# Kernel optimization log

Measured on AMD Instinct MI355X. Metric: run time of the kernel, lower is better.

Reference implementation:

```python
import jax, jax.numpy as jnp
import numpy as np

D_MODEL = 1024
EXPERT_DIM = 2048
N_EXPERTS = 8
LN_EPS = 1e-5


def _bit_quant(W):
    # W: [out, in] (or [..., out, in]); per-output-row ternary quantization with STE
    scale = jnp.clip(jnp.mean(jnp.abs(W), axis=-1, keepdims=True), 1e-5, None)
    w_q = jnp.clip(jnp.round(W / scale), -1.0, 1.0) * scale
    return W + jax.lax.stop_gradient(w_q - W)


def setup_inputs() -> dict:
    key = jax.random.key(0)
    ks = jax.random.split(key, 7)
    x = jax.random.normal(ks[0], (4, 2048, D_MODEL), dtype=jnp.float32)
    # kaiming_normal fan_out, linear -> std = 1/sqrt(out_features)
    shared_w1 = jax.random.normal(ks[1], (EXPERT_DIM, D_MODEL), dtype=jnp.float32) / np.sqrt(EXPERT_DIM)
    shared_w2 = jax.random.normal(ks[2], (D_MODEL, EXPERT_DIM), dtype=jnp.float32) / np.sqrt(D_MODEL)
    expert_w1 = jax.random.normal(ks[3], (N_EXPERTS, EXPERT_DIM, D_MODEL), dtype=jnp.float32) / np.sqrt(EXPERT_DIM)
    expert_w2 = jax.random.normal(ks[4], (N_EXPERTS, D_MODEL, EXPERT_DIM), dtype=jnp.float32) / np.sqrt(D_MODEL)
    router_w = 0.02 * jax.random.normal(ks[5], (N_EXPERTS, D_MODEL), dtype=jnp.float32)
    ln_gamma = jnp.ones((D_MODEL,), dtype=jnp.float32)
    ln_beta = jnp.zeros((D_MODEL,), dtype=jnp.float32)
    return {"x": x, "shared_w1": shared_w1, "shared_w2": shared_w2,
            "expert_w1": expert_w1, "expert_w2": expert_w2,
            "router_w": router_w, "ln_gamma": ln_gamma, "ln_beta": ln_beta}


def reference(x, shared_w1, shared_w2, expert_w1, expert_w2, router_w, ln_gamma, ln_beta):
    # LayerNorm
    mu = jnp.mean(x, axis=-1, keepdims=True)
    var = jnp.mean(jnp.square(x - mu), axis=-1, keepdims=True)
    h = (x - mu) / jnp.sqrt(var + LN_EPS) * ln_gamma + ln_beta  # [B,T,D]

    # Shared expert (BitLinear -> SiLU -> BitLinear)
    sw1, sw2 = _bit_quant(shared_w1), _bit_quant(shared_w2)
    shared_out = jax.nn.silu(jnp.einsum('btd,fd->btf', h, sw1)) @ sw2.T  # [B,T,D]

    # Top-1 router
    probs = jax.nn.softmax(h @ router_w.T, axis=-1)  # [B,T,E]
    top_prob = jnp.max(probs, axis=-1)               # [B,T]
    top_idx = jnp.argmax(probs, axis=-1)             # [B,T]

    # Routed experts: compute all experts densely, select via one-hot gate
    ew1, ew2 = _bit_quant(expert_w1), _bit_quant(expert_w2)
    h1 = jax.nn.silu(jnp.einsum('btd,efd->ebtf', h, ew1))      # [E,B,T,F]
    eo = jnp.einsum('ebtf,edf->ebtd', h1, ew2)                 # [E,B,T,D]
    gate = jax.nn.one_hot(top_idx, N_EXPERTS, dtype=h.dtype) * top_prob[..., None]  # [B,T,E]
    routed_out = jnp.einsum('ebtd,bte->btd', eo, gate)

    return shared_out + routed_out
```

## Files before the change

### kernel.cpp

```cpp
#include <hip/hip_runtime.h>
#include <hip/hip_bf16.h>

#define D_MODEL 1024
#define F_DIM   2048
#define NE      8
#define NTOK    8192
#define MAXT    72
#define HBLK    32

typedef __attribute__((ext_vector_type(8))) short bf16x8;
typedef __attribute__((ext_vector_type(4))) float f32x4;

__device__ __forceinline__ unsigned short f2b(float f) {
    unsigned int u = __float_as_uint(f);
    u += 0x7FFFu + ((u >> 16) & 1u);
    return (unsigned short)(u >> 16);
}
__device__ __forceinline__ unsigned int pack2(float a, float b) {
    return (unsigned int)f2b(a) | ((unsigned int)f2b(b) << 16);
}
__device__ __forceinline__ void async16(const void* g, void* l) {
    __builtin_amdgcn_global_load_lds((const __attribute__((address_space(1))) void*)g,
                                     (__attribute__((address_space(3))) void*)l, 16, 0, 0);
}

template <int K>
__global__ __launch_bounds__(256) void quant_rows(const float* __restrict__ W,
                                                  unsigned short* __restrict__ Q) {
    constexpr int PER = K / 256;
    constexpr int PV  = PER / 4;
    __shared__ float sred[4];
    const int tid = threadIdx.x;
    const size_t row = blockIdx.x;
    const float4* Wv = (const float4*)(W + row * (size_t)K) + tid * PV;
    float4 v[PV];
#pragma unroll
    for (int i = 0; i < PV; i++) v[i] = Wv[i];
    float s = 0.f;
#pragma unroll
    for (int i = 0; i < PV; i++)
        s += fabsf(v[i].x) + fabsf(v[i].y) + fabsf(v[i].z) + fabsf(v[i].w);
#pragma unroll
    for (int o = 32; o > 0; o >>= 1) s += __shfl_down(s, o);
    if ((tid & 63) == 0) sred[tid >> 6] = s;
    __syncthreads();
    float scale = (sred[0] + sred[1] + sred[2] + sred[3]) * (1.0f / K);
    scale = fmaxf(scale, 1e-5f);
    const float inv = 1.0f / scale;
    unsigned int* Qu = (unsigned int*)(Q + row * (size_t)K) + tid * (PER / 2);
#pragma unroll
    for (int i = 0; i < PV; i++) {
        float q0 = fminf(1.f, fmaxf(-1.f, rintf(v[i].x * inv))) * scale;
        float q1 = fminf(1.f, fmaxf(-1.f, rintf(v[i].y * inv))) * scale;
        float q2 = fminf(1.f, fmaxf(-1.f, rintf(v[i].z * inv))) * scale;
        float q3 = fminf(1.f, fmaxf(-1.f, rintf(v[i].w * inv))) * scale;
        Qu[2 * i]     = pack2(q0, q1);
        Qu[2 * i + 1] = pack2(q2, q3);
    }
}

__global__ __launch_bounds__(256) void ln_router(const float* __restrict__ x,
                                                 const float* __restrict__ gamma,
                                                 const float* __restrict__ beta,
                                                 const float* __restrict__ rw,
                                                 unsigned short* __restrict__ h,
                                                 int* __restrict__ top_idx,
                                                 float* __restrict__ top_prob) {
    const int lane = threadIdx.x & 63;
    const size_t tok = blockIdx.x * 4 + (threadIdx.x >> 6);

    const float4* xr = (const float4*)(x + tok * D_MODEL);
    float4 xv[4];
#pragma unroll
    for (int i = 0; i < 4; i++) xv[i] = xr[lane + 64 * i];
    float s = 0.f, q = 0.f;
#pragma unroll
    for (int i = 0; i < 4; i++) {
        s += xv[i].x + xv[i].y + xv[i].z + xv[i].w;
        q += xv[i].x * xv[i].x + xv[i].y * xv[i].y + xv[i].z * xv[i].z + xv[i].w * xv[i].w;
    }
#pragma unroll
    for (int o = 32; o > 0; o >>= 1) { s += __shfl_down(s, o); q += __shfl_down(q, o); }
    s = __shfl(s, 0); q = __shfl(q, 0);
    const float mean = s * (1.0f / D_MODEL);
    const float rstd = rsqrtf(q * (1.0f / D_MODEL) - mean * mean + 1e-5f);

    float4 hv[4];
    unsigned int* hr = (unsigned int*)(h + tok * D_MODEL);
#pragma unroll
    for (int i = 0; i < 4; i++) {
        const float4 g  = ((const float4*)gamma)[lane + 64 * i];
        const float4 bt = ((const float4*)beta)[lane + 64 * i];
        hv[i].x = (xv[i].x - mean) * rstd * g.x + bt.x;
        hv[i].y = (xv[i].y - mean) * rstd * g.y + bt.y;
        hv[i].z = (xv[i].z - mean) * rstd * g.z + bt.z;
        hv[i].w = (xv[i].w - mean) * rstd * g.w + bt.w;
        hr[2 * (lane + 64 * i)]     = pack2(hv[i].x, hv[i].y);
        hr[2 * (lane + 64 * i) + 1] = pack2(hv[i].z, hv[i].w);
    }

    float acc[NE];
#pragma unroll
    for (int e = 0; e < NE; e++) {
        const float4* rr = (const float4*)(rw + e * D_MODEL);
        float a = 0.f;
#pragma unroll
        for (int i = 0; i < 4; i++) {
            const float4 r = rr[lane + 64 * i];
            a += hv[i].x * r.x + hv[i].y * r.y + hv[i].z * r.z + hv[i].w * r.w;
        }
        acc[e] = a;
    }
#pragma unroll
    for (int e = 0; e < NE; e++) {
#pragma unroll
        for (int o = 32; o > 0; o >>= 1) acc[e] += __shfl_down(acc[e], o);
    }
    if (lane == 0) {
        float m = acc[0]; int bi = 0;
#pragma unroll
        for (int e = 1; e < NE; e++) { if (acc[e] > m) { m = acc[e]; bi = e; } }
        float se = 0.f;
#pragma unroll
        for (int e = 0; e < NE; e++) se += __expf(acc[e] - m);
        top_idx[tok]  = bi;
        top_prob[tok] = 1.0f / se;
    }
}

__global__ __launch_bounds__(256) void hist_kernel(const int* __restrict__ top_idx,
                                                   int* __restrict__ blockhist) {
    __shared__ int lh[NE];
    if (threadIdx.x < NE) lh[threadIdx.x] = 0;
    __syncthreads();
    const int t = blockIdx.x * 256 + threadIdx.x;
    atomicAdd(&lh[top_idx[t]], 1);
    __syncthreads();
    if (threadIdx.x < NE) blockhist[blockIdx.x * NE + threadIdx.x] = lh[threadIdx.x];
}

__global__ __launch_bounds__(256) void scan_plan(const int* __restrict__ blockhist,
                                                 int* __restrict__ base,
                                                 int4* __restrict__ tilemap,
                                                 int* __restrict__ tok_perm) {
    __shared__ int sh[HBLK * NE];
    __shared__ int counts[NE];
    __shared__ int offsets[NE];
    __shared__ int tstart[NE + 1];
    const int tid = threadIdx.x;
    sh[tid] = blockhist[tid];
    __syncthreads();
    if (tid < NE) {
        int c = 0;
#pragma unroll
        for (int b = 0; b < HBLK; b++) c += sh[b * NE + tid];
        counts[tid] = c;
    }
    __syncthreads();
    if (tid == 0) {
        int off = 0, slot = 0;
#pragma unroll
        for (int e = 0; e < NE; e++) {
            offsets[e] = off;
            tstart[e] = slot;
            slot += (counts[e] + 127) >> 7;
            off += counts[e];
        }
        tstart[NE] = slot;
    }
    __syncthreads();
    if (tid < MAXT) {
        int4 t; t.x = 0; t.y = 0; t.z = 0; t.w = 0;
#pragma unroll
        for (int e = 0; e < NE; e++) {
            if (tid >= tstart[e] && tid < tstart[e + 1]) {
                const int k = (tid - tstart[e]) << 7;
                t.x = e; t.y = offsets[e] + k; t.z = min(128, counts[e] - k);
            }
        }
        tilemap[tid] = t;
    }
    {
        const int b = tid >> 3, e = tid & 7;
        int r = offsets[e];
        for (int bb = 0; bb < b; bb++) r += sh[bb * NE + e];
        base[b * NE + e] = r;
    }
    if (tid < 128) tok_perm[NTOK + tid] = 0;
}

__global__ __launch_bounds__(256) void scatter_tokens(const int* __restrict__ top_idx,
                                                      const float* __restrict__ top_prob,
                                                      const int* __restrict__ base,
                                                      int* __restrict__ tok_perm,
                                                      float* __restrict__ probg) {
    __shared__ int cur[NE];
    if (threadIdx.x < NE) cur[threadIdx.x] = base[blockIdx.x * NE + threadIdx.x];
    __syncthreads();
    const int t = blockIdx.x * 256 + threadIdx.x;
    const int e = top_idx[t];
    const int pos = atomicAdd(&cur[e], 1);
    tok_perm[pos] = t;
    probg[pos] = top_prob[t];
}

template <int EPI>
__global__ __launch_bounds__(256) void gemm_nt(const unsigned short* __restrict__ A,
                                               const unsigned short* __restrict__ Bw,
                                               void* __restrict__ Cv,
                                               int N, int K,
                                               const int4* __restrict__ tilemap,
                                               long long bstride,
                                               const int* __restrict__ tok_perm,
                                               const float* __restrict__ probg) {
    int m0, rowsValid;
    const unsigned short* B = Bw;
    if (EPI >= 2) {
        int4 tm = tilemap[blockIdx.y];
        rowsValid = tm.z;
        if (rowsValid == 0) return;
        m0 = tm.y;
        B += (size_t)tm.x * (size_t)bstride;
    } else {
        m0 = blockIdx.y * 128;
        rowsValid = 128;
    }
    const int n0 = blockIdx.x * 128;

    __shared__ unsigned short As[128 * 32];
    __shared__ unsigned short Bs[128 * 32];

    const int tid = threadIdx.x;
    const int lane = tid & 63;
    const int w = tid >> 6;
    const int wm = w >> 1, wn = w & 1;

    f32x4 acc[4][4];
#pragma unroll
    for (int i = 0; i < 4; i++)
#pragma unroll
        for (int j = 0; j < 4; j++) acc[i][j] = (f32x4){0.f, 0.f, 0.f, 0.f};

    const int rS = w * 16 + (lane >> 2);
    const int cS = (lane & 3) * 8;
    size_t ar0, ar1;
    if (EPI == 2) {
        ar0 = (size_t)tok_perm[m0 + rS] * (size_t)K;
        ar1 = (size_t)tok_perm[m0 + rS + 64] * (size_t)K;
    } else {
        ar0 = (size_t)(m0 + rS) * (size_t)K;
        ar1 = (size_t)(m0 + rS + 64) * (size_t)K;
    }
    const unsigned short* a0 = A + ar0 + cS;
    const unsigned short* a1 = A + ar1 + cS;
    const unsigned short* b0 = B + (size_t)(n0 + rS) * K + cS;
    const unsigned short* b1 = B + (size_t)(n0 + rS + 64) * K + cS;
    unsigned short* asl = As + w * 512;
    unsigned short* bsl = Bs + w * 512;

    const int fr = lane & 15, fq = lane >> 4;
    const bf16x8* Ar = (const bf16x8*)As;
    const bf16x8* Br = (const bf16x8*)Bs;
    const int aBase = (wm * 64 + fr) * 4 + fq;
    const int bBase = (wn * 64 + fr) * 4 + fq;

    for (int k0 = 0; k0 < K; k0 += 32) {
        async16(a0 + k0, asl);
        async16(a1 + k0, asl + 2048);
        async16(b0 + k0, bsl);
        async16(b1 + k0, bsl + 2048);
        __syncthreads();
        bf16x8 af[4], bfr[4];
#pragma unroll
        for (int i = 0; i < 4; i++) af[i] = Ar[aBase + i * 64];
#pragma unroll
        for (int j = 0; j < 4; j++) bfr[j] = Br[bBase + j * 64];
#pragma unroll
        for (int i = 0; i < 4; i++)
#pragma unroll
            for (int j = 0; j < 4; j++)
                acc[i][j] = __builtin_amdgcn_mfma_f32_16x16x32_bf16(af[i], bfr[j], acc[i][j], 0, 0, 0);
        __syncthreads();
    }

#pragma unroll
    for (int i = 0; i < 4; i++) {
        const int rb = wm * 64 + i * 16 + fq * 4;
#pragma unroll
        for (int t = 0; t < 4; t++) {
            const int r = rb + t;
            if (r < rowsValid) {
#pragma unroll
                for (int j = 0; j < 4; j++) {
                    const int c = n0 + wn * 64 + j * 16 + fr;
                    float v = acc[i][j][t];
                    if (EPI == 0 || EPI == 2) {
                        v = v / (1.0f + __expf(-v));
                        ((unsigned short*)Cv)[(size_t)(m0 + r) * N + c] = f2b(v);
                    } else if (EPI == 1) {
                        ((float*)Cv)[(size_t)(m0 + r) * N + c] = v;
                    } else {
                        const int tokr = tok_perm[m0 + r];
                        const float p = probg[m0 + r];
                        float* crow = (float*)Cv + (size_t)tokr * N;
                        crow[c] = crow[c] + p * v;
                    }
                }
            }
        }
    }
}

extern "C" void kernel_launch(void* const* d_in, const int* in_sizes, int n_in,
                              void* d_out, int out_size, void* d_ws, size_t ws_size,
                              hipStream_t stream) {
    const float* x   = (const float*)d_in[0];
    const float* sw1 = (const float*)d_in[1];
    const float* sw2 = (const float*)d_in[2];
    const float* ew1 = (const float*)d_in[3];
    const float* ew2 = (const float*)d_in[4];
    const float* rw  = (const float*)d_in[5];
    const float* gam = (const float*)d_in[6];
    const float* bet = (const float*)d_in[7];
    float* out = (float*)d_out;

    char* ws = (char*)d_ws;
    const size_t H_OFF    = 0;
    const size_t SW1Q_OFF = H_OFF + (size_t)NTOK * D_MODEL * 2;
    const size_t SW2Q_OFF = SW1Q_OFF + (size_t)F_DIM * D_MODEL * 2;
    const size_t EW1Q_OFF = SW2Q_OFF + (size_t)D_MODEL * F_DIM * 2;
    const size_t EW2Q_OFF = EW1Q_OFF + (size_t)NE * F_DIM * D_MODEL * 2;
    const size_t H1_OFF   = EW2Q_OFF + (size_t)NE * D_MODEL * F_DIM * 2;
    const size_t PERM_OFF = H1_OFF + (size_t)(NTOK + 128) * F_DIM * 2;
    const size_t PROBG_OFF = PERM_OFF + (NTOK + 128) * 4;
    const size_t IDX_OFF   = PROBG_OFF + NTOK * 4;
    const size_t PROB_OFF  = IDX_OFF + NTOK * 4;
    const size_t BH_OFF    = PROB_OFF + NTOK * 4;
    const size_t BASE_OFF  = BH_OFF + HBLK * NE * 4;
    const size_t TILE_OFF  = BASE_OFF + HBLK * NE * 4;

    unsigned short* h     = (unsigned short*)(ws + H_OFF);
    unsigned short* sw1q  = (unsigned short*)(ws + SW1Q_OFF);
    unsigned short* sw2q  = (unsigned short*)(ws + SW2Q_OFF);
    unsigned short* ew1q  = (unsigned short*)(ws + EW1Q_OFF);
    unsigned short* ew2q  = (unsigned short*)(ws + EW2Q_OFF);
    unsigned short* h1    = (unsigned short*)(ws + H1_OFF);
    int*   tok_perm = (int*)(ws + PERM_OFF);
    float* probg    = (float*)(ws + PROBG_OFF);
    int*   idx      = (int*)(ws + IDX_OFF);
    float* prob     = (float*)(ws + PROB_OFF);
    int*   blockhist = (int*)(ws + BH_OFF);
    int*   base      = (int*)(ws + BASE_OFF);
    int4*  tilemap   = (int4*)(ws + TILE_OFF);

    quant_rows<1024><<<2048, 256, 0, stream>>>(sw1, sw1q);
    quant_rows<2048><<<1024, 256, 0, stream>>>(sw2, sw2q);
    quant_rows<1024><<<16384, 256, 0, stream>>>(ew1, ew1q);
    quant_rows<2048><<<8192, 256, 0, stream>>>(ew2, ew2q);

    ln_router<<<NTOK / 4, 256, 0, stream>>>(x, gam, bet, rw, h, idx, prob);

    hist_kernel<<<HBLK, 256, 0, stream>>>(idx, blockhist);
    scan_plan<<<1, 256, 0, stream>>>(blockhist, base, tilemap, tok_perm);
    scatter_tokens<<<HBLK, 256, 0, stream>>>(idx, prob, base, tok_perm, probg);

    gemm_nt<0><<<dim3(F_DIM / 128, NTOK / 128), 256, 0, stream>>>(
        h, sw1q, h1, F_DIM, D_MODEL, nullptr, 0, nullptr, nullptr);
    gemm_nt<1><<<dim3(D_MODEL / 128, NTOK / 128), 256, 0, stream>>>(
        h1, sw2q, out, D_MODEL, F_DIM, nullptr, 0, nullptr, nullptr);

    gemm_nt<2><<<dim3(F_DIM / 128, MAXT), 256, 0, stream>>>(
        h, ew1q, h1, F_DIM, D_MODEL, tilemap, (long long)F_DIM * D_MODEL, tok_perm, nullptr);
    gemm_nt<3><<<dim3(D_MODEL / 128, MAXT), 256, 0, stream>>>(
        h1, ew2q, out, D_MODEL, F_DIM, tilemap, (long long)D_MODEL * F_DIM, tok_perm, probg);
}
```

Measured before the change: 493.8 us.

## Merge shared and expert up-projection GEMMs, use K=64 tiles with XOR-swizzled LDS

The shared and routed first-layer GEMMs now run in one launch by extending the grid: the first 64 row-blocks handle shared tokens and the rest handle expert tiles. Each writes into its own intermediate buffer. The K tile grows from 32 to 64 so every barrier pair covers twice as many MFMAs, and LDS uses an XOR swizzle to cut bank conflicts. The routed down-projection now writes the gated result directly, and the shared down-projection accumulates onto it afterwards. The cost is twice the LDS per block, which may lower occupancy, plus an extra intermediate buffer.

After: 446.9 us. -9.5%, faster.

```diff
diff --git a/kernel.cpp b/kernel.cpp
--- a/kernel.cpp
+++ b/kernel.cpp
@@ -204,31 +204,43 @@
     probg[pos] = top_prob[t];
 }
 
-template <int EPI>
-__global__ __launch_bounds__(256) void gemm_nt(const unsigned short* __restrict__ A,
-                                               const unsigned short* __restrict__ Bw,
-                                               void* __restrict__ Cv,
-                                               int N, int K,
-                                               const int4* __restrict__ tilemap,
-                                               long long bstride,
-                                               const int* __restrict__ tok_perm,
-                                               const float* __restrict__ probg) {
+template <int MODE>
+__global__ __launch_bounds__(256) void gemm64(const unsigned short* __restrict__ A,
+                                              const unsigned short* __restrict__ Bmain,
+                                              const unsigned short* __restrict__ Bexp,
+                                              unsigned short* __restrict__ C1s,
+                                              unsigned short* __restrict__ C1r,
+                                              float* __restrict__ Out,
+                                              int N, int K,
+                                              const int4* __restrict__ tilemap,
+                                              const int* __restrict__ tok_perm,
+                                              const float* __restrict__ probg) {
     int m0, rowsValid;
-    const unsigned short* B = Bw;
-    if (EPI >= 2) {
+    const unsigned short* B;
+    unsigned short* Cb = nullptr;
+    bool gather = false;
+    if (MODE == 0) {
+        if (blockIdx.y < 64) {
+            m0 = blockIdx.y * 128; rowsValid = 128; B = Bmain; Cb = C1s;
+        } else {
+            int4 tm = tilemap[blockIdx.y - 64];
+            if (tm.z == 0) return;
+            m0 = tm.y; rowsValid = tm.z;
+            B = Bexp + (size_t)tm.x * F_DIM * D_MODEL;
+            Cb = C1r; gather = true;
+        }
+    } else if (MODE == 1) {
         int4 tm = tilemap[blockIdx.y];
-        rowsValid = tm.z;
-        if (rowsValid == 0) return;
-        m0 = tm.y;
-        B += (size_t)tm.x * (size_t)bstride;
+        if (tm.z == 0) return;
+        m0 = tm.y; rowsValid = tm.z;
+        B = Bmain + (size_t)tm.x * D_MODEL * F_DIM;
     } else {
-        m0 = blockIdx.y * 128;
-        rowsValid = 128;
+        m0 = blockIdx.y * 128; rowsValid = 128; B = Bmain;
     }
     const int n0 = blockIdx.x * 128;
 
-    __shared__ unsigned short As[128 * 32];
-    __shared__ unsigned short Bs[128 * 32];
+    __shared__ unsigned short As[128 * 64];
+    __shared__ unsigned short Bs[128 * 64];
 
     const int tid = threadIdx.x;
     const int lane = tid & 63;
@@ -241,45 +253,51 @@
 #pragma unroll
         for (int j = 0; j < 4; j++) acc[i][j] = (f32x4){0.f, 0.f, 0.f, 0.f};
 
-    const int rS = w * 16 + (lane >> 2);
-    const int cS = (lane & 3) * 8;
-    size_t ar0, ar1;
-    if (EPI == 2) {
-        ar0 = (size_t)tok_perm[m0 + rS] * (size_t)K;
-        ar1 = (size_t)tok_perm[m0 + rS + 64] * (size_t)K;
-    } else {
-        ar0 = (size_t)(m0 + rS) * (size_t)K;
-        ar1 = (size_t)(m0 + rS + 64) * (size_t)K;
-    }
-    const unsigned short* a0 = A + ar0 + cS;
-    const unsigned short* a1 = A + ar1 + cS;
-    const unsigned short* b0 = B + (size_t)(n0 + rS) * K + cS;
-    const unsigned short* b1 = B + (size_t)(n0 + rS + 64) * K + cS;
-    unsigned short* asl = As + w * 512;
-    unsigned short* bsl = Bs + w * 512;
+    const int sRow = lane >> 3;
+    const int sCol = ((lane & 7) ^ sRow) * 8;
+    const unsigned short* aP[4];
+    const unsigned short* bP[4];
+#pragma unroll
+    for (int qq = 0; qq < 4; qq++) {
+        const int ra = w * 32 + qq * 8 + sRow;
+        size_t arow;
+        if (MODE == 0) arow = gather ? (size_t)tok_perm[m0 + ra] : (size_t)(m0 + ra);
+        else           arow = (size_t)(m0 + ra);
+        aP[qq] = A + arow * (size_t)K + sCol;
+        bP[qq] = B + (size_t)(n0 + ra) * K + sCol;
+    }
+    unsigned short* aL = As + w * 2048;
+    unsigned short* bL = Bs + w * 2048;
 
     const int fr = lane & 15, fq = lane >> 4;
     const bf16x8* Ar = (const bf16x8*)As;
     const bf16x8* Br = (const bf16x8*)Bs;
-    const int aBase = (wm * 64 + fr) * 4 + fq;
-    const int bBase = (wn * 64 + fr) * 4 + fq;
-
-    for (int k0 = 0; k0 < K; k0 += 32) {
-        async16(a0 + k0, asl);
-        async16(a1 + k0, asl + 2048);
-        async16(b0 + k0, bsl);
-        async16(b1 + k0, bsl + 2048);
+
+    for (int k0 = 0; k0 < K; k0 += 64) {
+#pragma unroll
+        for (int qq = 0; qq < 4; qq++) async16(aP[qq] + k0, aL + qq * 512);
+#pragma unroll
+        for (int qq = 0; qq < 4; qq++) async16(bP[qq] + k0, bL + qq * 512);
         __syncthreads();
-        bf16x8 af[4], bfr[4];
-#pragma unroll
-        for (int i = 0; i < 4; i++) af[i] = Ar[aBase + i * 64];
-#pragma unroll
-        for (int j = 0; j < 4; j++) bfr[j] = Br[bBase + j * 64];
-#pragma unroll
-        for (int i = 0; i < 4; i++)
-#pragma unroll
-            for (int j = 0; j < 4; j++)
-                acc[i][j] = __builtin_amdgcn_mfma_f32_16x16x32_bf16(af[i], bfr[j], acc[i][j], 0, 0, 0);
+#pragma unroll
+        for (int kc = 0; kc < 2; kc++) {
+            bf16x8 af[4], bf[4];
+#pragma unroll
+            for (int i = 0; i < 4; i++) {
+                const int row = wm * 64 + i * 16 + fr;
+                af[i] = Ar[row * 8 + (((kc << 2) + fq) ^ (fr & 7))];
+            }
+#pragma unroll
+            for (int j = 0; j < 4; j++) {
+                const int row = wn * 64 + j * 16 + fr;
+                bf[j] = Br[row * 8 + (((kc << 2) + fq) ^ (fr & 7))];
+            }
+#pragma unroll
+            for (int i = 0; i < 4; i++)
+#pragma unroll
+                for (int j = 0; j < 4; j++)
+                    acc[i][j] = __builtin_amdgcn_mfma_f32_16x16x32_bf16(af[i], bf[j], acc[i][j], 0, 0, 0);
+        }
         __syncthreads();
     }
 
@@ -294,16 +312,15 @@
                 for (int j = 0; j < 4; j++) {
                     const int c = n0 + wn * 64 + j * 16 + fr;
                     float v = acc[i][j][t];
-                    if (EPI == 0 || EPI == 2) {
+                    if (MODE == 0) {
                         v = v / (1.0f + __expf(-v));
-                        ((unsigned short*)Cv)[(size_t)(m0 + r) * N + c] = f2b(v);
-                    } else if (EPI == 1) {
-                        ((float*)Cv)[(size_t)(m0 + r) * N + c] = v;
+                        Cb[(size_t)(m0 + r) * N + c] = f2b(v);
+                    } else if (MODE == 1) {
+                        const int tokr = tok_perm[m0 + r];
+                        Out[(size_t)tokr * N + c] = probg[m0 + r] * v;
                     } else {
-                        const int tokr = tok_perm[m0 + r];
-                        const float p = probg[m0 + r];
-                        float* crow = (float*)Cv + (size_t)tokr * N;
-                        crow[c] = crow[c] + p * v;
+                        float* o = Out + (size_t)(m0 + r) * N + c;
+                        *o = *o + v;
                     }
                 }
             }
@@ -330,8 +347,9 @@
     const size_t SW2Q_OFF = SW1Q_OFF + (size_t)F_DIM * D_MODEL * 2;
     const size_t EW1Q_OFF = SW2Q_OFF + (size_t)D_MODEL * F_DIM * 2;
     const size_t EW2Q_OFF = EW1Q_OFF + (size_t)NE * F_DIM * D_MODEL * 2;
-    const size_t H1_OFF   = EW2Q_OFF + (size_t)NE * D_MODEL * F_DIM * 2;
-    const size_t PERM_OFF = H1_OFF + (size_t)(NTOK + 128) * F_DIM * 2;
+    const size_t H1S_OFF  = EW2Q_OFF + (size_t)NE * D_MODEL * F_DIM * 2;
+    const size_t H1R_OFF  = H1S_OFF + (size_t)NTOK * F_DIM * 2;
+    const size_t PERM_OFF = H1R_OFF + (size_t)(NTOK + 128) * F_DIM * 2;
     const size_t PROBG_OFF = PERM_OFF + (NTOK + 128) * 4;
     const size_t IDX_OFF   = PROBG_OFF + NTOK * 4;
     const size_t PROB_OFF  = IDX_OFF + NTOK * 4;
@@ -344,7 +362,8 @@
     unsigned short* sw2q  = (unsigned short*)(ws + SW2Q_OFF);
     unsigned short* ew1q  = (unsigned short*)(ws + EW1Q_OFF);
     unsigned short* ew2q  = (unsigned short*)(ws + EW2Q_OFF);
-    unsigned short* h1    = (unsigned short*)(ws + H1_OFF);
+    unsigned short* h1s   = (unsigned short*)(ws + H1S_OFF);
+    unsigned short* h1r   = (unsigned short*)(ws + H1R_OFF);
     int*   tok_perm = (int*)(ws + PERM_OFF);
     float* probg    = (float*)(ws + PROBG_OFF);
     int*   idx      = (int*)(ws + IDX_OFF);
@@ -364,13 +383,11 @@
     scan_plan<<<1, 256, 0, stream>>>(blockhist, base, tilemap, tok_perm);
     scatter_tokens<<<HBLK, 256, 0, stream>>>(idx, prob, base, tok_perm, probg);
 
-    gemm_nt<0><<<dim3(F_DIM / 128, NTOK / 128), 256, 0, stream>>>(
-        h, sw1q, h1, F_DIM, D_MODEL, nullptr, 0, nullptr, nullptr);
-    gemm_nt<1><<<dim3(D_MODEL / 128, NTOK / 128), 256, 0, stream>>>(
-        h1, sw2q, out, D_MODEL, F_DIM, nullptr, 0, nullptr, nullptr);
-
-    gemm_nt<2><<<dim3(F_DIM / 128, MAXT), 256, 0, stream>>>(
-        h, ew1q, h1, F_DIM, D_MODEL, tilemap, (long long)F_DIM * D_MODEL, tok_perm, nullptr);
-    gemm_nt<3><<<dim3(D_MODEL / 128, MAXT), 256, 0, stream>>>(
-        h1, ew2q, out, D_MODEL, F_DIM, tilemap, (long long)D_MODEL * F_DIM, tok_perm, probg);
-}
+    gemm64<0><<<dim3(F_DIM / 128, 64 + MAXT), 256, 0, stream>>>(
+        h, sw1q, ew1q, h1s, h1r, nullptr, F_DIM, D_MODEL, tilemap, tok_perm, nullptr);
+
+    gemm64<1><<<dim3(D_MODEL / 128, MAXT), 256, 0, stream>>>(
+        h1r, ew2q, nullptr, nullptr, nullptr, out, D_MODEL, F_DIM, tilemap, tok_perm, probg);
+    gemm64<2><<<dim3(D_MODEL / 128, NTOK / 128), 256, 0, stream>>>(
+        h1s, sw2q, nullptr, nullptr, nullptr, out, D_MODEL, F_DIM, tilemap, tok_perm, probg);
+}
```
